# Performance work log

Hardware: AMD Instinct MI355X
Metric: run time of the kernel (lower is better)

## Reference

```python
import jax, jax.numpy as jnp
import numpy as np


def setup_inputs() -> dict:
    key = jax.random.key(0)
    B = 64          # number of utterances (segments)
    N = 16384       # total frames = sum(segment_num)
    D = 1024        # embedding_size
    A = 2048        # attention_dim
    H = 8           # attention_head_num
    k1, k2, k3, k4 = jax.random.split(key, 4)
    # ragged segment lengths, all >= 1, summing exactly to N
    rng = np.random.default_rng(0)
    lens = rng.integers(64, 512, size=B).astype(np.float64)
    lens = np.maximum(1, (lens * N / lens.sum()).astype(np.int64))
    lens[-1] += N - lens.sum()
    assert lens.sum() == N and (lens > 0).all()
    segment_num = jnp.asarray(lens, dtype=jnp.int32)
    x = jax.random.normal(k1, (N, D), jnp.float32)
    # torch Linear weights, stored pre-transposed as [in, out]
    w1 = jax.random.normal(k2, (D, A), jnp.float32) / np.sqrt(D)
    w2 = jax.random.normal(k3, (A, H), jnp.float32) / np.sqrt(A)
    # post_fc: Linear(D*H -> D, bias=False), stored as [D*H, D]
    w_post = jax.random.normal(k4, (D * H, D), jnp.float32) / np.sqrt(D * H)
    return {"x": x, "segment_num": segment_num, "w1": w1, "w2": w2, "w_post": w_post}


def reference(x, segment_num, w1, w2, w_post):
    N, D = x.shape
    B = segment_num.shape[0]
    H = w2.shape[1]
    # segment id for every frame (ragged -> flat segment ids)
    seg_ids = jnp.repeat(jnp.arange(B), segment_num, total_repeat_length=N)  # [N]

    # MultiAtt.w1: Linear -> ReLU -> Linear, per frame
    h = jnp.maximum(x @ w1, 0.0) @ w2  # [N, H]

    # per-segment softmax over the time axis (dim 0 within each segment)
    m = jax.ops.segment_max(h, seg_ids, num_segments=B)          # [B, H]
    p = jnp.exp(h - m[seg_ids])                                  # [N, H]
    s = jax.ops.segment_sum(p, seg_ids, num_segments=B)          # [B, H]
    attn = p / s[seg_ids]                                        # [N, H]

    # per-segment x^T @ attn -> [B, D, H] (matches torch.mm(x.T, attn))
    out_bdh = jax.ops.segment_sum(x[:, :, None] * attn[:, None, :], seg_ids, num_segments=B)
    # flatten row-major over (D, H) like out.view(-1), then post_fc (no bias)
    out = out_bdh.reshape(B, D * H) @ w_post                     # [B, D]

    # attn_i = attn^T @ attn per segment -> [B, H, H]
    attn_gram = jax.ops.segment_sum(attn[:, :, None] * attn[:, None, :], seg_ids, num_segments=B)

    # segment_type == 'average': per-segment mean of frames -> [B, D]
    out_segment = jax.ops.segment_sum(x, seg_ids, num_segments=B) / segment_num[:, None].astype(x.dtype)

    return out, out_segment, attn_gram
```

## Files before the change

### kernel.cpp

```cpp
#include <hip/hip_runtime.h>
#include <hip/hip_bf16.h>

#define NB 64
#define NN 16384
#define ND 1024
#define NA 2048
#define NH 8
#define KSPL 64
#define NPL 16
#define MAXL 1024

typedef __attribute__((ext_vector_type(4))) float f32x4;
typedef __attribute__((ext_vector_type(8))) short short8;
typedef __attribute__((ext_vector_type(8))) unsigned short ushort8;

__device__ __forceinline__ unsigned short f2bf(float f) {
    unsigned int u = __float_as_uint(f);
    u = (u + 0x7fff + ((u >> 16) & 1)) >> 16;
    return (unsigned short)u;
}

__device__ __forceinline__ float bf2f(unsigned short s) {
    return __uint_as_float((unsigned int)s << 16);
}

__device__ __forceinline__ void load_lds16(const void* g, void* l) {
    __builtin_amdgcn_global_load_lds((const __attribute__((address_space(1))) void*)g,
                                     (__attribute__((address_space(3))) void*)l, 16, 0, 0);
}

__device__ __forceinline__ void hsum_row(const float* __restrict__ h_part, int n, float* v) {
#pragma unroll
    for (int q = 0; q < NH; q++) v[q] = 0.f;
#pragma unroll
    for (int p = 0; p < NPL; p++) {
        const float4* hp = (const float4*)(h_part + (size_t)p * (NN * NH) + (size_t)n * NH);
        float4 u0 = hp[0], u1 = hp[1];
        v[0] += u0.x; v[1] += u0.y; v[2] += u0.z; v[3] += u0.w;
        v[4] += u1.x; v[5] += u1.y; v[6] += u1.z; v[7] += u1.w;
    }
}

__global__ __launch_bounds__(256) void k_pre(const float* __restrict__ x,
                                             const float* __restrict__ w1,
                                             const int* __restrict__ segnum,
                                             unsigned short* __restrict__ xb,
                                             unsigned short* __restrict__ w1t,
                                             int* __restrict__ segoff) {
    __shared__ unsigned short t[32][33];
    const int bx = blockIdx.x;
    if (bx < 8192) {
        size_t i = ((size_t)bx * 256 + threadIdx.x) * 8;
        float4 a = *(const float4*)(x + i);
        float4 b = *(const float4*)(x + i + 4);
        ushort8 o;
        o[0] = f2bf(a.x); o[1] = f2bf(a.y); o[2] = f2bf(a.z); o[3] = f2bf(a.w);
        o[4] = f2bf(b.x); o[5] = f2bf(b.y); o[6] = f2bf(b.z); o[7] = f2bf(b.w);
        *(ushort8*)(xb + i) = o;
    } else if (bx < 10240) {
        const int idx = bx - 8192;
        const int a0 = (idx & 63) * 32, d0 = (idx >> 6) * 32;
        const int tx = threadIdx.x & 31, ty4 = (threadIdx.x >> 5) * 4;
#pragma unroll
        for (int i = 0; i < 4; i++)
            t[tx][ty4 + i] = f2bf(w1[(size_t)(d0 + ty4 + i) * NA + a0 + tx]);
        __syncthreads();
#pragma unroll
        for (int i = 0; i < 4; i++)
            w1t[(size_t)(a0 + ty4 + i) * ND + d0 + tx] = t[ty4 + i][tx];
    } else {
        if (threadIdx.x == 0) {
            int a = 0;
            segoff[0] = 0;
            for (int b = 0; b < NB; b++) { a += segnum[b]; segoff[b + 1] = a; }
        }
    }
}

__global__ __launch_bounds__(256) void k_c1h(const unsigned short* __restrict__ xb,
                                             const unsigned short* __restrict__ w1t,
                                             const float* __restrict__ w2,
                                             float* __restrict__ h_part) {
    __shared__ unsigned short SM[21760];
    unsigned short* As  = SM;
    unsigned short* Bs  = SM + 8192;
    unsigned short* c1s = SM;
    unsigned short* w2hi = SM + 17408;
    unsigned short* w2lo = SM + 19584;

    const int tid = threadIdx.x;
    const int wave = tid >> 6, lane = tid & 63;
    const int wm = wave & 1, wn = wave >> 1;
    const int m0 = blockIdx.x * 128, n0 = blockIdx.y * 128;
    const int quad = lane >> 4, lc = lane & 15;

    for (int i = tid; i < 2176; i += 256) { w2hi[i] = 0; w2lo[i] = 0; }
    for (int i = tid; i < 1024; i += 256) {
        int k = i >> 3, q = i & 7;
        float w = w2[(size_t)(n0 + k) * NH + q];
        unsigned short hi = f2bf(w);
        w2hi[q * 136 + k] = hi;
        w2lo[q * 136 + k] = f2bf(w - bf2f(hi));
    }

    f32x4 acc[4][4];
#pragma unroll
    for (int i = 0; i < 4; i++)
#pragma unroll
        for (int j = 0; j < 4; j++) acc[i][j] = (f32x4){0.f, 0.f, 0.f, 0.f};

    const int srow = lane >> 3;
    const int sg = lane & 7;

    for (int k0 = 0; k0 < ND; k0 += 64) {
        __syncthreads();
#pragma unroll
        for (int i = 0; i < 4; i++) {
            int r = wave * 32 + i * 8 + srow;
            int gc = (sg ^ (r & 7)) * 8;
            load_lds16(xb + (size_t)(m0 + r) * ND + k0 + gc, As + r * 64 + sg * 8);
            load_lds16(w1t + (size_t)(n0 + r) * ND + k0 + gc, Bs + r * 64 + sg * 8);
        }
        __syncthreads();
#pragma unroll
        for (int ksub = 0; ksub < 2; ksub++) {
            short8 af[4], bf[4];
            const int lg = ksub * 4 + quad;
#pragma unroll
            for (int t = 0; t < 4; t++) {
                int m = wm * 64 + t * 16 + lc;
                af[t] = *(const short8*)&As[m * 64 + (lg ^ (m & 7)) * 8];
                int n = wn * 64 + t * 16 + lc;
                bf[t] = *(const short8*)&Bs[n * 64 + (lg ^ (n & 7)) * 8];
            }
#pragma unroll
            for (int mi = 0; mi < 4; mi++)
#pragma unroll
                for (int ni = 0; ni < 4; ni++)
                    acc[mi][ni] = __builtin_amdgcn_mfma_f32_16x16x32_bf16(
                        af[mi], bf[ni], acc[mi][ni], 0, 0, 0);
        }
    }

    __syncthreads();
#pragma unroll
    for (int mi = 0; mi < 4; mi++)
#pragma unroll
        for (int ni = 0; ni < 4; ni++) {
            const int col = wn * 64 + ni * 16 + lc;
#pragma unroll
            for (int r = 0; r < 4; r++) {
                const int row = wm * 64 + mi * 16 + quad * 4 + r;
                c1s[row * 136 + col] = f2bf(fmaxf(acc[mi][ni][r], 0.f));
            }
        }
    __syncthreads();

    f32x4 hacc[2];
    hacc[0] = (f32x4){0.f, 0.f, 0.f, 0.f};
    hacc[1] = (f32x4){0.f, 0.f, 0.f, 0.f};
#pragma unroll
    for (int ks = 0; ks < 4; ks++) {
        short8 bh = *(const short8*)&w2hi[lc * 136 + ks * 32 + quad * 8];
        short8 bl = *(const short8*)&w2lo[lc * 136 + ks * 32 + quad * 8];
#pragma unroll
        for (int mt = 0; mt < 2; mt++) {
            short8 af = *(const short8*)&c1s[(wave * 32 + mt * 16 + lc) * 136 + ks * 32 + quad * 8];
            hacc[mt] = __builtin_amdgcn_mfma_f32_16x16x32_bf16(af, bh, hacc[mt], 0, 0, 0);
            hacc[mt] = __builtin_amdgcn_mfma_f32_16x16x32_bf16(af, bl, hacc[mt], 0, 0, 0);
        }
    }

    if (lc < NH) {
        float* hp = h_part + (size_t)blockIdx.y * (NN * NH);
#pragma unroll
        for (int mt = 0; mt < 2; mt++)
#pragma unroll
            for (int r = 0; r < 4; r++)
                hp[(size_t)(m0 + wave * 32 + mt * 16 + quad * 4 + r) * NH + lc] = hacc[mt][r];
    }
}

__global__ __launch_bounds__(256) void k_seg(const float* __restrict__ h_part,
                                             const unsigned short* __restrict__ xb,
                                             const int* __restrict__ segoff,
                                             float* __restrict__ bdh,
                                             float* __restrict__ out_segment,
                                             float* __restrict__ gram) {
    const int dc = blockIdx.x;
    const int b  = blockIdx.y;
    const int s0 = segoff[b], s1 = segoff[b + 1];
    const int len = s1 - s0;
    const int cap = len < MAXL ? len : MAXL;
    const int tid = threadIdx.x;
    const int wv = tid >> 6;

    __shared__ float hl[MAXL * NH];
    __shared__ float redf[8 * 32 * 33];
    __shared__ float xsred[8][132];
    __shared__ float red[4][NH], mb[NH], sinv[NH], gred[4][64];

    for (int i = tid; i < cap * 2; i += 256) {
        float4 s = make_float4(0.f, 0.f, 0.f, 0.f);
#pragma unroll
        for (int p = 0; p < NPL; p++) {
            float4 u = *((const float4*)(h_part + (size_t)p * (NN * NH)) + (size_t)s0 * 2 + i);
            s.x += u.x; s.y += u.y; s.z += u.z; s.w += u.w;
        }
        ((float4*)hl)[i] = s;
    }
    __syncthreads();

    float mx[NH];
#pragma unroll
    for (int q = 0; q < NH; q++) mx[q] = -1e30f;
    for (int r = tid; r < len; r += 256) {
        float v[NH];
        if (r < MAXL) {
#pragma unroll
            for (int q = 0; q < NH; q++) v[q] = hl[r * NH + q];
        } else hsum_row(h_part, s0 + r, v);
#pragma unroll
        for (int q = 0; q < NH; q++) mx[q] = fmaxf(mx[q], v[q]);
    }
#pragma unroll
    for (int q = 0; q < NH; q++)
        for (int o = 1; o < 64; o <<= 1) mx[q] = fmaxf(mx[q], __shfl_xor(mx[q], o));
    if ((tid & 63) == 0)
        for (int q = 0; q < NH; q++) red[wv][q] = mx[q];
    __syncthreads();
    if (tid < NH)
        mb[tid] = fmaxf(fmaxf(red[0][tid], red[1][tid]), fmaxf(red[2][tid], red[3][tid]));
    __syncthreads();

    float sm[NH];
#pragma unroll
    for (int q = 0; q < NH; q++) sm[q] = 0.f;
    for (int r = tid; r < len; r += 256) {
        float v[NH];
        if (r < MAXL) {
#pragma unroll
            for (int q = 0; q < NH; q++) v[q] = hl[r * NH + q];
        } else hsum_row(h_part, s0 + r, v);
#pragma unroll
        for (int q = 0; q < NH; q++) sm[q] += expf(v[q] - mb[q]);
    }
#pragma unroll
    for (int q = 0; q < NH; q++)
        for (int o = 1; o < 64; o <<= 1) sm[q] += __shfl_xor(sm[q], o);
    if ((tid & 63) == 0)
        for (int q = 0; q < NH; q++) red[wv][q] = sm[q];
    __syncthreads();
    if (tid < NH)
        sinv[tid] = 1.0f / (red[0][tid] + red[1][tid] + red[2][tid] + red[3][tid]);
    __syncthreads();

    for (int r = tid; r < cap; r += 256) {
#pragma unroll
        for (int q = 0; q < NH; q++)
            hl[r * NH + q] = expf(hl[r * NH + q] - mb[q]) * sinv[q];
    }
    __syncthreads();

    if (dc == 0) {
        float g[NH][NH];
#pragma unroll
        for (int i = 0; i < NH; i++)
#pragma unroll
            for (int j = 0; j < NH; j++) g[i][j] = 0.f;
        for (int r = tid; r < len; r += 256) {
            float a[NH];
            if (r < MAXL) {
#pragma unroll
                for (int q = 0; q < NH; q++) a[q] = hl[r * NH + q];
            } else {
                hsum_row(h_part, s0 + r, a);
#pragma unroll
                for (int q = 0; q < NH; q++) a[q] = expf(a[q] - mb[q]) * sinv[q];
            }
#pragma unroll
            for (int i = 0; i < NH; i++)
#pragma unroll
                for (int j = 0; j < NH; j++) g[i][j] += a[i] * a[j];
        }
#pragma unroll
        for (int i = 0; i < NH; i++)
#pragma unroll
            for (int j = 0; j < NH; j++)
                for (int o = 1; o < 64; o <<= 1) g[i][j] += __shfl_xor(g[i][j], o);
        if ((tid & 63) == 0) {
#pragma unroll
            for (int i = 0; i < NH; i++)
#pragma unroll
                for (int j = 0; j < NH; j++) gred[wv][i * NH + j] = g[i][j];
        }
        __syncthreads();
        if (tid < 64)
            gram[(size_t)b * 64 + tid] = gred[0][tid] + gred[1][tid] + gred[2][tid] + gred[3][tid];
    }

    const int fo = tid >> 5, dg = tid & 31;
    const int d = dc * 128 + dg * 4;
    float acc[4][NH];
    float xs4[4] = {0.f, 0.f, 0.f, 0.f};
#pragma unroll
    for (int dd = 0; dd < 4; dd++)
#pragma unroll
        for (int q = 0; q < NH; q++) acc[dd][q] = 0.f;

    for (int n = fo; n < len; n += 8) {
        ushort4 xv = *(const ushort4*)(xb + (size_t)(s0 + n) * ND + d);
        float a[NH];
        if (n < MAXL) {
            const float4* ap = (const float4*)&hl[n * NH];
            float4 a0 = ap[0], a1 = ap[1];
            a[0] = a0.x; a[1] = a0.y; a[2] = a0.z; a[3] = a0.w;
            a[4] = a1.x; a[5] = a1.y; a[6] = a1.z; a[7] = a1.w;
        } else {
            hsum_row(h_part, s0 + n, a);
#pragma unroll
            for (int q = 0; q < NH; q++) a[q] = expf(a[q] - mb[q]) * sinv[q];
        }
        float xf[4] = {bf2f(xv.x), bf2f(xv.y), bf2f(xv.z), bf2f(xv.w)};
#pragma unroll
        for (int dd = 0; dd < 4; dd++) {
            xs4[dd] += xf[dd];
#pragma unroll
            for (int q = 0; q < NH; q++) acc[dd][q] += xf[dd] * a[q];
        }
    }

    {
        float* rp = redf + (fo * 32 + dg) * 33;
#pragma unroll
        for (int dd = 0; dd < 4; dd++)
#pragma unroll
            for (int q = 0; q < NH; q++) rp[dd * 8 + q] = acc[dd][q];
#pragma unroll
        for (int dd = 0; dd < 4; dd++) xsred[fo][dg * 4 + dd] = xs4[dd];
    }
    __syncthreads();
    {
        float ov[4];
#pragma unroll
        for (int j = 0; j < 4; j++) {
            int o = tid * 4 + j;
            int g = o >> 5, e = o & 31;
            float s = 0.f;
#pragma unroll
            for (int f = 0; f < 8; f++) s += redf[(f * 32 + g) * 33 + e];
            ov[j] = s;
        }
        *(float4*)(bdh + (size_t)b * (ND * NH) + (size_t)dc * 1024 + tid * 4) =
            make_float4(ov[0], ov[1], ov[2], ov[3]);
        if (tid < 128) {
            float s = 0.f;
#pragma unroll
            for (int f = 0; f < 8; f++) s += xsred[f][tid];
            out_segment[(size_t)b * ND + dc * 128 + tid] = s / (float)len;
        }
    }
}

__global__ __launch_bounds__(256) void k_post(const float* __restrict__ bdh,
                                              const float* __restrict__ wp,
                                              float* __restrict__ out_part) {
    __shared__ float as[32][68];
    __shared__ float bs[32][128];
    const int tid = threadIdx.x;
    const int n0 = blockIdx.x * 128;
    const int k0 = blockIdx.y * (8192 / KSPL);
    const int tr = tid >> 4, tc = tid & 15;

    float acc[4][8];
#pragma unroll
    for (int i = 0; i < 4; i++)
#pragma unroll
        for (int j = 0; j < 8; j++) acc[i][j] = 0.f;

    for (int kc = 0; kc < 8192 / KSPL; kc += 32) {
        __syncthreads();
        {
            int r = tid >> 2;
            int c = (tid & 3) * 8;
            const float4* gp = (const float4*)(bdh + (size_t)r * (ND * NH) + k0 + kc + c);
            float4 v0 = gp[0], v1 = gp[1];
            as[c + 0][r] = v0.x; as[c + 1][r] = v0.y; as[c + 2][r] = v0.z; as[c + 3][r] = v0.w;
            as[c + 4][r] = v1.x; as[c + 5][r] = v1.y; as[c + 6][r] = v1.z; as[c + 7][r] = v1.w;
        }
        {
            int r = tid >> 3;
            int c = (tid & 7) * 16;
            const float4* gp = (const float4*)(wp + (size_t)(k0 + kc + r) * ND + n0 + c);
            float4* sp = (float4*)&bs[r][c];
            sp[0] = gp[0]; sp[1] = gp[1]; sp[2] = gp[2]; sp[3] = gp[3];
        }
        __syncthreads();
#pragma unroll
        for (int k = 0; k < 32; k++) {
            float4 a  = *(const float4*)&as[k][tr * 4];
            float4 b0 = *(const float4*)&bs[k][tc * 8];
            float4 b1 = *(const float4*)&bs[k][tc * 8 + 4];
            float av[4] = {a.x, a.y, a.z, a.w};
            float bv[8] = {b0.x, b0.y, b0.z, b0.w, b1.x, b1.y, b1.z, b1.w};
#pragma unroll
            for (int i = 0; i < 4; i++)
#pragma unroll
                for (int j = 0; j < 8; j++) acc[i][j] += av[i] * bv[j];
        }
    }

    float* op = out_part + (size_t)blockIdx.y * (NB * ND);
#pragma unroll
    for (int i = 0; i < 4; i++)
#pragma unroll
        for (int j = 0; j < 8; j++)
            op[(size_t)(tr * 4 + i) * ND + n0 + tc * 8 + j] = acc[i][j];
}

__global__ __launch_bounds__(256) void k_post_red(const float* __restrict__ out_part,
                                                  float* __restrict__ out) {
    const int i = (blockIdx.x * 256 + threadIdx.x) * 4;
    float4 s = *(const float4*)(out_part + i);
#pragma unroll
    for (int p = 1; p < KSPL; p++) {
        float4 v = *(const float4*)(out_part + (size_t)p * (NB * ND) + i);
        s.x += v.x; s.y += v.y; s.z += v.z; s.w += v.w;
    }
    *(float4*)(out + i) = s;
}

extern "C" void kernel_launch(void* const* d_in, const int* in_sizes, int n_in,
                              void* d_out, int out_size, void* d_ws, size_t ws_size,
                              hipStream_t stream) {
    (void)in_sizes; (void)n_in; (void)out_size; (void)ws_size;
    const float* x      = (const float*)d_in[0];
    const int*   segnum = (const int*)d_in[1];
    const float* w1     = (const float*)d_in[2];
    const float* w2     = (const float*)d_in[3];
    const float* wpost  = (const float*)d_in[4];

    float* out         = (float*)d_out;
    float* out_segment = out + NB * ND;
    float* gram        = out + 2 * NB * ND;

    char* ws = (char*)d_ws;
    const size_t MB = 1024 * 1024;
    int*   segoff   = (int*)ws;
    float* bdh      = (float*)(ws + 2 * MB);
    float* h_part   = (float*)(ws + 4 * MB);
    unsigned short* xb  = (unsigned short*)(ws + 12 * MB);
    unsigned short* w1t = (unsigned short*)(ws + 44 * MB);
    float* out_part  = (float*)(ws + 48 * MB);

    k_pre<<<10241, 256, 0, stream>>>(x, w1, segnum, xb, w1t, segoff);
    k_c1h<<<dim3(NN / 128, NA / 128), 256, 0, stream>>>(xb, w1t, w2, h_part);
    k_seg<<<dim3(8, NB), 256, 0, stream>>>(h_part, xb, segoff, bdh, out_segment, gram);
    k_post<<<dim3(ND / 128, KSPL), 256, 0, stream>>>(bdh, wpost, out_part);
    k_post_red<<<(NB * ND) / (256 * 4), 256, 0, stream>>>(out_part, out);
}
```

Measured before the change: 284.7 us.

## Fuse post split-K reduction via last-block atomic, remap GEMM blocks per XCD

The separate split-K reduction kernel is folded into k_post: each column tile counts finished K-slices with an atomic, and the last block sums the partials. KSPL is halved, so there are fewer partials to write and read. The main GEMM grid is flattened and remapped so that blocks on the same XCD share M rows, aiming for better L2 reuse. The w1 transpose now uses 64x64 tiles with vectorized stores. The changes add a memset launch and a serialized tail reduction, and the w1 transpose tile stores element-wise into LDS with possible bank conflicts.

```diff
diff --git a/kernel.cpp b/kernel.cpp
--- a/kernel.cpp
+++ b/kernel.cpp
@@ -6,7 +6,7 @@
 #define ND 1024
 #define NA 2048
 #define NH 8
-#define KSPL 64
+#define KSPL 32
 #define NPL 16
 #define MAXL 1024
 
@@ -47,29 +47,33 @@
                                              unsigned short* __restrict__ xb,
                                              unsigned short* __restrict__ w1t,
                                              int* __restrict__ segoff) {
-    __shared__ unsigned short t[32][33];
+    __shared__ unsigned short t2[64][68];
     const int bx = blockIdx.x;
+    const int tid = threadIdx.x;
     if (bx < 8192) {
-        size_t i = ((size_t)bx * 256 + threadIdx.x) * 8;
+        size_t i = ((size_t)bx * 256 + tid) * 8;
         float4 a = *(const float4*)(x + i);
         float4 b = *(const float4*)(x + i + 4);
         ushort8 o;
         o[0] = f2bf(a.x); o[1] = f2bf(a.y); o[2] = f2bf(a.z); o[3] = f2bf(a.w);
         o[4] = f2bf(b.x); o[5] = f2bf(b.y); o[6] = f2bf(b.z); o[7] = f2bf(b.w);
         *(ushort8*)(xb + i) = o;
-    } else if (bx < 10240) {
+    } else if (bx < 8192 + 512) {
         const int idx = bx - 8192;
-        const int a0 = (idx & 63) * 32, d0 = (idx >> 6) * 32;
-        const int tx = threadIdx.x & 31, ty4 = (threadIdx.x >> 5) * 4;
-#pragma unroll
-        for (int i = 0; i < 4; i++)
-            t[tx][ty4 + i] = f2bf(w1[(size_t)(d0 + ty4 + i) * NA + a0 + tx]);
-        __syncthreads();
-#pragma unroll
-        for (int i = 0; i < 4; i++)
-            w1t[(size_t)(a0 + ty4 + i) * ND + d0 + tx] = t[ty4 + i][tx];
+        const int a0 = (idx & 31) * 64, d0 = (idx >> 5) * 64;
+        for (int i = tid; i < 64 * 64; i += 256) {
+            int d = i >> 6, a = i & 63;
+            t2[a][d] = f2bf(w1[(size_t)(d0 + d) * NA + a0 + a]);
+        }
+        __syncthreads();
+        for (int i = tid; i < 64 * 16; i += 256) {
+            int r = i >> 4, c4 = (i & 15) * 4;
+            ushort4 v;
+            v.x = t2[r][c4]; v.y = t2[r][c4 + 1]; v.z = t2[r][c4 + 2]; v.w = t2[r][c4 + 3];
+            *(ushort4*)&w1t[(size_t)(a0 + r) * ND + d0 + c4] = v;
+        }
     } else {
-        if (threadIdx.x == 0) {
+        if (tid == 0) {
             int a = 0;
             segoff[0] = 0;
             for (int b = 0; b < NB; b++) { a += segnum[b]; segoff[b + 1] = a; }
@@ -88,10 +92,15 @@
     unsigned short* w2hi = SM + 17408;
     unsigned short* w2lo = SM + 19584;
 
+    const int L = blockIdx.x;
+    const int xcd = L & 7, j = L >> 3;
+    const int mIdx = xcd * 16 + (j >> 4);
+    const int nIdx = j & 15;
+    const int m0 = mIdx * 128, n0 = nIdx * 128;
+
     const int tid = threadIdx.x;
     const int wave = tid >> 6, lane = tid & 63;
     const int wm = wave & 1, wn = wave >> 1;
-    const int m0 = blockIdx.x * 128, n0 = blockIdx.y * 128;
     const int quad = lane >> 4, lc = lane & 15;
 
     for (int i = tid; i < 2176; i += 256) { w2hi[i] = 0; w2lo[i] = 0; }
@@ -107,7 +116,7 @@
 #pragma unroll
     for (int i = 0; i < 4; i++)
 #pragma unroll
-        for (int j = 0; j < 4; j++) acc[i][j] = (f32x4){0.f, 0.f, 0.f, 0.f};
+        for (int j2 = 0; j2 < 4; j2++) acc[i][j2] = (f32x4){0.f, 0.f, 0.f, 0.f};
 
     const int srow = lane >> 3;
     const int sg = lane & 7;
@@ -172,7 +181,7 @@
     }
 
     if (lc < NH) {
-        float* hp = h_part + (size_t)blockIdx.y * (NN * NH);
+        float* hp = h_part + (size_t)nIdx * (NN * NH);
 #pragma unroll
         for (int mt = 0; mt < 2; mt++)
 #pragma unroll
@@ -364,9 +373,12 @@
 
 __global__ __launch_bounds__(256) void k_post(const float* __restrict__ bdh,
                                               const float* __restrict__ wp,
-                                              float* __restrict__ out_part) {
+                                              float* __restrict__ out_part,
+                                              float* __restrict__ out,
+                                              int* __restrict__ pcount) {
     __shared__ float as[32][68];
     __shared__ float bs[32][128];
+    __shared__ int isLast;
     const int tid = threadIdx.x;
     const int n0 = blockIdx.x * 128;
     const int k0 = blockIdx.y * (8192 / KSPL);
@@ -416,18 +428,27 @@
 #pragma unroll
         for (int j = 0; j < 8; j++)
             op[(size_t)(tr * 4 + i) * ND + n0 + tc * 8 + j] = acc[i][j];
-}
-
-__global__ __launch_bounds__(256) void k_post_red(const float* __restrict__ out_part,
-                                                  float* __restrict__ out) {
-    const int i = (blockIdx.x * 256 + threadIdx.x) * 4;
-    float4 s = *(const float4*)(out_part + i);
-#pragma unroll
-    for (int p = 1; p < KSPL; p++) {
-        float4 v = *(const float4*)(out_part + (size_t)p * (NB * ND) + i);
-        s.x += v.x; s.y += v.y; s.z += v.z; s.w += v.w;
-    }
-    *(float4*)(out + i) = s;
+
+    __threadfence();
+    __syncthreads();
+    if (tid == 0)
+        isLast = (atomicAdd(&pcount[blockIdx.x], 1) == KSPL - 1);
+    __syncthreads();
+    if (isLast) {
+        __threadfence();
+#pragma unroll
+        for (int j = 0; j < 8; j++) {
+            int v = tid + j * 256;
+            int r = v >> 5, c4 = (v & 31) * 4;
+            float4 s = make_float4(0.f, 0.f, 0.f, 0.f);
+            for (int p = 0; p < KSPL; p++) {
+                float4 u = *(const float4*)(out_part + (size_t)p * (NB * ND) +
+                                            (size_t)r * ND + n0 + c4);
+                s.x += u.x; s.y += u.y; s.z += u.z; s.w += u.w;
+            }
+            *(float4*)(out + (size_t)r * ND + n0 + c4) = s;
+        }
+    }
 }
 
 extern "C" void kernel_launch(void* const* d_in, const int* in_sizes, int n_in,
@@ -447,15 +468,16 @@
     char* ws = (char*)d_ws;
     const size_t MB = 1024 * 1024;
     int*   segoff   = (int*)ws;
+    int*   pcount   = (int*)(ws + 1024);
     float* bdh      = (float*)(ws + 2 * MB);
     float* h_part   = (float*)(ws + 4 * MB);
     unsigned short* xb  = (unsigned short*)(ws + 12 * MB);
     unsigned short* w1t = (unsigned short*)(ws + 44 * MB);
     float* out_part  = (float*)(ws + 48 * MB);
 
-    k_pre<<<10241, 256, 0, stream>>>(x, w1, segnum, xb, w1t, segoff);
-    k_c1h<<<dim3(NN / 128, NA / 128), 256, 0, stream>>>(xb, w1t, w2, h_part);
+    hipMemsetAsync(pcount, 0, 8 * sizeof(int), stream);
+    k_pre<<<8192 + 512 + 1, 256, 0, stream>>>(x, w1, segnum, xb, w1t, segoff);
+    k_c1h<<<2048, 256, 0, stream>>>(xb, w1t, w2, h_part);
     k_seg<<<dim3(8, NB), 256, 0, stream>>>(h_part, xb, segoff, bdh, out_segment, gram);
-    k_post<<<dim3(ND / 128, KSPL), 256, 0, stream>>>(bdh, wpost, out_part);
-    k_post_red<<<(NB * ND) / (256 * 4), 256, 0, stream>>>(out_part, out);
-}
+    k_post<<<dim3(ND / 128, KSPL), 256, 0, stream>>>(bdh, wpost, out_part, out, pcount);
+}
```

New measurement: 346.9 us. +21.9%, slower.
